# Performance work log

Measured on AMD Instinct MI355X. Metric: run time of the kernel, lower is better.

The kernel has to match this reference:

```python
import jax, jax.numpy as jnp
import numpy as np

GROUPS = 1024
K_N = 32
FEAT_DIM = 64
EPS = 1e-05


def farthest_point_sample(xyz, npoint):
    # xyz: [B, N, 3] -> centroids [B, npoint] int32
    # Original torch code starts from a random point; we use index 0 for determinism.
    B, N, _ = xyz.shape

    def step(carry, _):
        distance, farthest = carry
        centroid = jnp.take_along_axis(xyz, farthest[:, None, None], axis=1)  # [B,1,3]
        dist = jnp.sum((xyz - centroid) ** 2, axis=-1)  # [B,N]
        distance = jnp.minimum(distance, dist)
        new_far = jnp.argmax(distance, axis=-1).astype(jnp.int32)
        return (distance, new_far), farthest

    init = (jnp.full((B, N), 1e10, dtype=xyz.dtype), jnp.zeros((B,), jnp.int32))
    _, cents = jax.lax.scan(step, init, None, length=npoint)
    return cents.T  # [B, npoint]


def index_points(points, idx):
    # points: [B, N, C]; idx: [B, ...] -> [B, ..., C]
    B = points.shape[0]
    bidx = jnp.arange(B).reshape((B,) + (1,) * (idx.ndim - 1))
    return points[bidx, idx]


def square_distance(src, dst):
    # src [B,S,C], dst [B,N,C] -> [B,S,N]
    d = -2.0 * jnp.einsum('bsc,bnc->bsn', src, dst)
    d = d + jnp.sum(src ** 2, -1)[:, :, None]
    d = d + jnp.sum(dst ** 2, -1)[:, None, :]
    return d


def setup_inputs() -> dict:
    key = jax.random.key(0)
    k1, k2 = jax.random.split(key)
    xyz = jax.random.normal(k1, (8, 3, 4096), dtype=jnp.float32)
    feats = jax.random.normal(k2, (8, FEAT_DIM, 4096), dtype=jnp.float32)
    affine_alpha_p = jnp.ones((1, 1, 1, FEAT_DIM), jnp.float32)
    affine_beta_p = jnp.zeros((1, 1, 1, FEAT_DIM), jnp.float32)
    return {"xyz": xyz, "feats": feats,
            "affine_alpha_p": affine_alpha_p, "affine_beta_p": affine_beta_p}


def reference(xyz, feats, affine_alpha_p, affine_beta_p):
    xyz = jnp.transpose(xyz, (0, 2, 1))      # [B,N,3]
    feats = jnp.transpose(feats, (0, 2, 1))  # [B,N,D]
    B, N, _ = xyz.shape
    S, k = GROUPS, K_N

    fps_idx = farthest_point_sample(xyz, S)          # [B,S]
    new_xyz = index_points(xyz, fps_idx)             # [B,S,3]
    new_feats = index_points(feats, fps_idx)         # [B,S,D]

    sqr = square_distance(new_xyz, xyz)              # [B,S,N]
    _, idx = jax.lax.top_k(-sqr, k)                  # smallest-k -> [B,S,k]
    grouped = index_points(feats, idx)               # [B,S,k,D]

    mean = new_feats[:, :, None, :]                  # [B,S,1,D]
    diff = grouped - mean
    # torch.std over flattened per-batch, unbiased (ddof=1)
    std = jnp.std(diff.reshape(B, -1), axis=-1, ddof=1)[:, None, None, None]
    grouped = diff / (std + EPS)
    grouped = affine_alpha_p * grouped + affine_beta_p

    point_feats = jnp.concatenate(
        [grouped, grouped - new_feats[:, :, None, :]], axis=-1)  # [B,S,k,2D]

    new_feats_out = jnp.transpose(new_feats, (0, 2, 1))          # [B,D,S]
    new_xyz_out = jnp.transpose(new_xyz, (0, 2, 1))              # [B,3,S]
    point_feats_out = jnp.transpose(point_feats, (0, 3, 1, 2))   # [B,2D,S,k]
    return (new_xyz_out, new_feats_out, point_feats_out)
```

## Files before the change

### kernel.cpp

```cpp
#include <hip/hip_runtime.h>

#define NPTS 4096
#define NSAMP 1024
#define KNN_K 32
#define FDIM 64
#define EPSF 1e-5f

typedef float v2f __attribute__((ext_vector_type(2)));

#define DPP_MAX64(CTRL)                                                          \
  {                                                                              \
    unsigned _olo = (unsigned)__builtin_amdgcn_update_dpp(0, (int)klo, CTRL,     \
                                                          0xf, 0xf, true);       \
    unsigned _ohi = (unsigned)__builtin_amdgcn_update_dpp(0, (int)khi, CTRL,     \
                                                          0xf, 0xf, true);       \
    unsigned long long _ok = ((unsigned long long)_ohi << 32) | _olo;            \
    unsigned long long _ck = ((unsigned long long)khi << 32) | klo;              \
    if (_ok > _ck) { klo = _olo; khi = _ohi; }                                   \
  }

__global__ __launch_bounds__(512) void fps_kernel(const float* __restrict__ xyz,
                                                  int* __restrict__ fps_idx,
                                                  float* __restrict__ sqnorm,
                                                  float* __restrict__ out0,
                                                  float4* __restrict__ nx4) {
#pragma clang fp contract(off)
  __shared__ float4 pts[NPTS];
  __shared__ unsigned long long skeys[2][8];
  __shared__ int fpsb[NSAMP];
  const int b = blockIdx.x, t = threadIdx.x;
  const int lane = t & 63, w = t >> 6;
  const float* xb = xyz + (size_t)b * 3 * NPTS;
  v2f px[4], py[4], pz[4], dst[4];
#pragma unroll
  for (int j = 0; j < 4; ++j) {
    int p0 = (2 * j) * 512 + t, p1 = (2 * j + 1) * 512 + t;
    float x0 = xb[p0], y0 = xb[NPTS + p0], z0 = xb[2 * NPTS + p0];
    float x1 = xb[p1], y1 = xb[NPTS + p1], z1 = xb[2 * NPTS + p1];
    float sq0 = __fadd_rn(__fadd_rn(__fmul_rn(x0, x0), __fmul_rn(y0, y0)),
                          __fmul_rn(z0, z0));
    float sq1 = __fadd_rn(__fadd_rn(__fmul_rn(x1, x1), __fmul_rn(y1, y1)),
                          __fmul_rn(z1, z1));
    pts[p0] = make_float4(x0, y0, z0, sq0);
    pts[p1] = make_float4(x1, y1, z1, sq1);
    sqnorm[b * NPTS + p0] = sq0;
    sqnorm[b * NPTS + p1] = sq1;
    px[j].x = x0; px[j].y = x1;
    py[j].x = y0; py[j].y = y1;
    pz[j].x = z0; pz[j].y = z1;
    dst[j].x = 1e10f;
    dst[j].y = 1e10f;
  }
  if (t == 0) { fps_idx[b * NSAMP] = 0; fpsb[0] = 0; }
  __syncthreads();
  float4 c = pts[0];
  for (int it = 1; it < NSAMP; ++it) {
    v2f vcx, vcy, vcz;
    vcx.x = c.x; vcx.y = c.x;
    vcy.x = c.y; vcy.y = c.y;
    vcz.x = c.z; vcz.y = c.z;
#pragma unroll
    for (int j = 0; j < 4; ++j) {
      v2f dx = px[j] - vcx;
      v2f dy = py[j] - vcy;
      v2f dz = pz[j] - vcz;
      v2f dd = (dx * dx + dy * dy) + dz * dz;
      dst[j].x = fminf(dst[j].x, dd.x);
      dst[j].y = fminf(dst[j].y, dd.y);
    }
    float bv = -1.0f;
    int bi = 0;
#pragma unroll
    for (int k = 0; k < 8; ++k) {
      float nd = (k & 1) ? dst[k >> 1].y : dst[k >> 1].x;
      int n = k * 512 + t;
      if (nd > bv) { bv = nd; bi = n; }
    }
    unsigned bvb = __float_as_uint(bv);
    unsigned klo = (bvb << 12) | (unsigned)(4095 - bi);
    unsigned khi = bvb >> 20;
    DPP_MAX64(0x111)
    DPP_MAX64(0x112)
    DPP_MAX64(0x114)
    DPP_MAX64(0x118)
    DPP_MAX64(0x142)
    DPP_MAX64(0x143)
    const int buf = it & 1;
    if (lane == 63) skeys[buf][w] = ((unsigned long long)khi << 32) | klo;
    __syncthreads();
    unsigned long long kk = skeys[buf][lane & 7];
    klo = (unsigned)kk;
    khi = (unsigned)(kk >> 32);
    DPP_MAX64(0x111)
    DPP_MAX64(0x112)
    DPP_MAX64(0x114)
    unsigned flo = (unsigned)__builtin_amdgcn_readlane((int)klo, 7);
    int far = 4095 - (int)(flo & 0xfffu);
    if (t == 0) { fps_idx[b * NSAMP + it] = far; fpsb[it] = far; }
    c = pts[far];
  }
  __syncthreads();
#pragma unroll
  for (int k = 0; k < 2; ++k) {
    int s = k * 512 + t;
    int p = fpsb[s];
    float4 q = pts[p];
    out0[(b * 3 + 0) * 1024 + s] = q.x;
    out0[(b * 3 + 1) * 1024 + s] = q.y;
    out0[(b * 3 + 2) * 1024 + s] = q.z;
    nx4[b * 1024 + s] = q;
  }
}

__global__ __launch_bounds__(256) void gather_feats_kernel(const float* __restrict__ feats,
                                                           const int* __restrict__ fps,
                                                           float* __restrict__ out1,
                                                           float* __restrict__ nf) {
  int i = blockIdx.x * 256 + threadIdx.x;
  int s = i & 1023, c = (i >> 10) & 63, b = i >> 16;
  int p = fps[(b << 10) + s];
  float v = feats[((size_t)(b * 64 + c)) * NPTS + p];
  out1[(b * 64 + c) * 1024 + s] = v;
  nf[(((b << 10) + s) << 6) + c] = v;
}

__device__ __forceinline__ unsigned long long mk_key(float xn, float yn, float zn,
                                                     float sq, float cx, float cy,
                                                     float cz, float src2, int n) {
  float dot = __fmaf_rn(zn, cz, __fmaf_rn(yn, cy, __fmul_rn(xn, cx)));
  float d = __fadd_rn(__fadd_rn(__fmul_rn(-2.0f, dot), src2), sq);
  unsigned mb = __float_as_uint(d);
  mb = (mb & 0x80000000u) ? ~mb : (mb | 0x80000000u);
  return ((unsigned long long)mb << 32) | (unsigned)n;
}

__global__ __launch_bounds__(256, 2) void knn_kernel(const float* __restrict__ xyz,
                                                     const float* __restrict__ sqnorm,
                                                     const float4* __restrict__ nx4,
                                                     int* __restrict__ knn) {
  const int lane = threadIdx.x & 63;
  const int w = threadIdx.x >> 6;
  const int row = blockIdx.x * 4 + w;
  const int b = row >> 10;
  const float4 c4 = nx4[row];
  const float cx = c4.x, cy = c4.y, cz = c4.z, src2 = c4.w;
  const float4* x4 = (const float4*)(xyz + (size_t)b * 3 * NPTS);
  const float4* y4 = (const float4*)(xyz + (size_t)b * 3 * NPTS + NPTS);
  const float4* z4 = (const float4*)(xyz + (size_t)b * 3 * NPTS + 2 * NPTS);
  const float4* s4 = (const float4*)(sqnorm + (size_t)b * NPTS);
  unsigned long long key[64];
#pragma unroll
  for (int jj = 0; jj < 16; ++jj) {
    int vi = jj * 64 + lane;
    float4 xv = x4[vi], yv = y4[vi], zv = z4[vi], sv = s4[vi];
    int n0 = vi * 4;
    key[jj * 4 + 0] = mk_key(xv.x, yv.x, zv.x, sv.x, cx, cy, cz, src2, n0);
    key[jj * 4 + 1] = mk_key(xv.y, yv.y, zv.y, sv.y, cx, cy, cz, src2, n0 + 1);
    key[jj * 4 + 2] = mk_key(xv.z, yv.z, zv.z, sv.z, cx, cy, cz, src2, n0 + 2);
    key[jj * 4 + 3] = mk_key(xv.w, yv.w, zv.w, sv.w, cx, cy, cz, src2, n0 + 3);
  }
  unsigned long long last = 0ull;
  const int out_base = row * KNN_K;
#pragma unroll 1
  for (int r = 0; r < KNN_K; ++r) {
    unsigned long long cur = ~0ull;
#pragma unroll
    for (int j = 0; j < 64; ++j) {
      unsigned long long k = key[j];
      if (k > last && k < cur) cur = k;
    }
#pragma unroll
    for (int off = 32; off > 0; off >>= 1) {
      unsigned long long o = __shfl_xor(cur, off);
      cur = (o < cur) ? o : cur;
    }
    last = cur;
    if (lane == r) knn[out_base + r] = (int)(unsigned)(cur & 0xffffffffull);
  }
}

__global__ __launch_bounds__(256) void stats_kernel(const float* __restrict__ feats,
                                                    const float* __restrict__ nf,
                                                    const int* __restrict__ knn,
                                                    double* __restrict__ stats) {
  const int b = blockIdx.x >> 5;
  const int chunk = blockIdx.x & 31;
  const int base = chunk * 65536;
  double sm = 0.0, sq = 0.0;
  for (int i = 0; i < 256; ++i) {
    int e = base + i * 256 + threadIdx.x;
    int c = e >> 15;
    int sk = e & 32767;
    int s = sk >> 5, j = sk & 31;
    int p = knn[((((b << 10) + s)) << 5) + j];
    float f = feats[((size_t)(b * 64 + c)) * NPTS + p];
    float m = nf[(((b << 10) + s) << 6) + c];
    double d = (double)__fsub_rn(f, m);
    sm += d;
    sq += d * d;
  }
#pragma unroll
  for (int off = 32; off > 0; off >>= 1) {
    sm += __shfl_down(sm, off);
    sq += __shfl_down(sq, off);
  }
  __shared__ double red[8];
  int w = threadIdx.x >> 6;
  if ((threadIdx.x & 63) == 0) { red[w * 2] = sm; red[w * 2 + 1] = sq; }
  __syncthreads();
  if (threadIdx.x == 0) {
    atomicAdd(&stats[b * 2 + 0], red[0] + red[2] + red[4] + red[6]);
    atomicAdd(&stats[b * 2 + 1], red[1] + red[3] + red[5] + red[7]);
  }
}

__global__ __launch_bounds__(256) void out_kernel(const float* __restrict__ feats,
                                                  const float* __restrict__ nf,
                                                  const int* __restrict__ knn,
                                                  const double* __restrict__ stats,
                                                  const float* __restrict__ alpha,
                                                  const float* __restrict__ beta,
                                                  float* __restrict__ out2) {
  const int plane = blockIdx.x;
  const int b = plane >> 6, c = plane & 63;
  const int sk = blockIdx.y * 256 + threadIdx.x;
  const int s = sk >> 5, j = sk & 31;
  const double n = 2097152.0;
  double sm = stats[b * 2], sqs = stats[b * 2 + 1];
  double var = (sqs - sm * sm / n) / (n - 1.0);
  float stdf = (float)sqrt(var);
  float denom = stdf + EPSF;
  int p = knn[((((b << 10) + s)) << 5) + j];
  float f = feats[((size_t)(b * 64 + c)) * NPTS + p];
  float m = nf[(((b << 10) + s) << 6) + c];
  float diff = __fsub_rn(f, m);
  float g = alpha[c] * (diff / denom) + beta[c];
  size_t o1 = (((size_t)(b * 128 + c) << 10) + (size_t)s) * 32 + j;
  size_t o2 = (((size_t)(b * 128 + 64 + c) << 10) + (size_t)s) * 32 + j;
  out2[o1] = g;
  out2[o2] = g - m;
}

extern "C" void kernel_launch(void* const* d_in, const int* in_sizes, int n_in,
                              void* d_out, int out_size, void* d_ws, size_t ws_size,
                              hipStream_t stream) {
  (void)in_sizes; (void)n_in; (void)out_size; (void)ws_size;
  const float* xyz   = (const float*)d_in[0];
  const float* feats = (const float*)d_in[1];
  const float* alpha = (const float*)d_in[2];
  const float* beta  = (const float*)d_in[3];
  float* out  = (float*)d_out;
  float* out0 = out;
  float* out1 = out + 24576;
  float* out2 = out + 24576 + 524288;

  char* ws = (char*)d_ws;
  int*    fps   = (int*)ws;
  float*  sqn   = (float*)(ws + 32768);
  float4* nx4   = (float4*)(ws + 163840);
  float*  nf    = (float*)(ws + 294912);
  int*    knn   = (int*)(ws + 2392064);
  double* stats = (double*)(ws + 3440640);

  hipMemsetAsync(stats, 0, 128, stream);
  fps_kernel<<<8, 512, 0, stream>>>(xyz, fps, sqn, out0, nx4);
  gather_feats_kernel<<<2048, 256, 0, stream>>>(feats, fps, out1, nf);
  knn_kernel<<<2048, 256, 0, stream>>>(xyz, sqn, nx4, knn);
  stats_kernel<<<256, 256, 0, stream>>>(feats, nf, knn, stats);
  out_kernel<<<dim3(512, 128), 256, 0, stream>>>(feats, nf, knn, stats, alpha, beta, out2);
}
```

Measured before the change: 977.0 us.

## Merge knn and feature gather into one launch, vectorize stats and output kernels

Merges the feature-gather kernel into the knn kernel as extra blocks so there is one fewer launch and the gather can overlap with knn work. Vectorizes the gather, stats and output kernels to handle four elements per thread with int4/float4 loads and stores, and replaces the per-element divide with a reciprocal multiply. The stats kernel now accumulates per thread in float rather than double before the double reduction, which may change numerical accuracy. The knn kernel also drops its launch_bounds minimum of two blocks per CU, which can change register allocation and occupancy.

```diff
diff --git a/kernel.cpp b/kernel.cpp
--- a/kernel.cpp
+++ b/kernel.cpp
@@ -112,18 +112,6 @@
   }
 }
 
-__global__ __launch_bounds__(256) void gather_feats_kernel(const float* __restrict__ feats,
-                                                           const int* __restrict__ fps,
-                                                           float* __restrict__ out1,
-                                                           float* __restrict__ nf) {
-  int i = blockIdx.x * 256 + threadIdx.x;
-  int s = i & 1023, c = (i >> 10) & 63, b = i >> 16;
-  int p = fps[(b << 10) + s];
-  float v = feats[((size_t)(b * 64 + c)) * NPTS + p];
-  out1[(b * 64 + c) * 1024 + s] = v;
-  nf[(((b << 10) + s) << 6) + c] = v;
-}
-
 __device__ __forceinline__ unsigned long long mk_key(float xn, float yn, float zn,
                                                      float sq, float cx, float cy,
                                                      float cz, float src2, int n) {
@@ -134,48 +122,66 @@
   return ((unsigned long long)mb << 32) | (unsigned)n;
 }
 
-__global__ __launch_bounds__(256, 2) void knn_kernel(const float* __restrict__ xyz,
-                                                     const float* __restrict__ sqnorm,
-                                                     const float4* __restrict__ nx4,
-                                                     int* __restrict__ knn) {
-  const int lane = threadIdx.x & 63;
-  const int w = threadIdx.x >> 6;
-  const int row = blockIdx.x * 4 + w;
-  const int b = row >> 10;
-  const float4 c4 = nx4[row];
-  const float cx = c4.x, cy = c4.y, cz = c4.z, src2 = c4.w;
-  const float4* x4 = (const float4*)(xyz + (size_t)b * 3 * NPTS);
-  const float4* y4 = (const float4*)(xyz + (size_t)b * 3 * NPTS + NPTS);
-  const float4* z4 = (const float4*)(xyz + (size_t)b * 3 * NPTS + 2 * NPTS);
-  const float4* s4 = (const float4*)(sqnorm + (size_t)b * NPTS);
-  unsigned long long key[64];
-#pragma unroll
-  for (int jj = 0; jj < 16; ++jj) {
-    int vi = jj * 64 + lane;
-    float4 xv = x4[vi], yv = y4[vi], zv = z4[vi], sv = s4[vi];
-    int n0 = vi * 4;
-    key[jj * 4 + 0] = mk_key(xv.x, yv.x, zv.x, sv.x, cx, cy, cz, src2, n0);
-    key[jj * 4 + 1] = mk_key(xv.y, yv.y, zv.y, sv.y, cx, cy, cz, src2, n0 + 1);
-    key[jj * 4 + 2] = mk_key(xv.z, yv.z, zv.z, sv.z, cx, cy, cz, src2, n0 + 2);
-    key[jj * 4 + 3] = mk_key(xv.w, yv.w, zv.w, sv.w, cx, cy, cz, src2, n0 + 3);
-  }
-  unsigned long long last = 0ull;
-  const int out_base = row * KNN_K;
+__global__ __launch_bounds__(256) void mid_kernel(const float* __restrict__ xyz,
+                                                  const float* __restrict__ sqnorm,
+                                                  const float4* __restrict__ nx4,
+                                                  int* __restrict__ knn,
+                                                  const float* __restrict__ feats,
+                                                  const int* __restrict__ fps,
+                                                  float* __restrict__ out1,
+                                                  float* __restrict__ nf) {
+  if (blockIdx.x < 2048) {
+    const int lane = threadIdx.x & 63;
+    const int w = threadIdx.x >> 6;
+    const int row = blockIdx.x * 4 + w;
+    const int b = row >> 10;
+    const float4 c4 = nx4[row];
+    const float cx = c4.x, cy = c4.y, cz = c4.z, src2 = c4.w;
+    const float4* x4 = (const float4*)(xyz + (size_t)b * 3 * NPTS);
+    const float4* y4 = (const float4*)(xyz + (size_t)b * 3 * NPTS + NPTS);
+    const float4* z4 = (const float4*)(xyz + (size_t)b * 3 * NPTS + 2 * NPTS);
+    const float4* s4 = (const float4*)(sqnorm + (size_t)b * NPTS);
+    unsigned long long key[64];
+#pragma unroll
+    for (int jj = 0; jj < 16; ++jj) {
+      int vi = jj * 64 + lane;
+      float4 xv = x4[vi], yv = y4[vi], zv = z4[vi], sv = s4[vi];
+      int n0 = vi * 4;
+      key[jj * 4 + 0] = mk_key(xv.x, yv.x, zv.x, sv.x, cx, cy, cz, src2, n0);
+      key[jj * 4 + 1] = mk_key(xv.y, yv.y, zv.y, sv.y, cx, cy, cz, src2, n0 + 1);
+      key[jj * 4 + 2] = mk_key(xv.z, yv.z, zv.z, sv.z, cx, cy, cz, src2, n0 + 2);
+      key[jj * 4 + 3] = mk_key(xv.w, yv.w, zv.w, sv.w, cx, cy, cz, src2, n0 + 3);
+    }
+    unsigned long long last = 0ull;
+    const int out_base = row * KNN_K;
 #pragma unroll 1
-  for (int r = 0; r < KNN_K; ++r) {
-    unsigned long long cur = ~0ull;
-#pragma unroll
-    for (int j = 0; j < 64; ++j) {
-      unsigned long long k = key[j];
-      if (k > last && k < cur) cur = k;
-    }
-#pragma unroll
-    for (int off = 32; off > 0; off >>= 1) {
-      unsigned long long o = __shfl_xor(cur, off);
-      cur = (o < cur) ? o : cur;
-    }
-    last = cur;
-    if (lane == r) knn[out_base + r] = (int)(unsigned)(cur & 0xffffffffull);
+    for (int r = 0; r < KNN_K; ++r) {
+      unsigned long long cur = ~0ull;
+#pragma unroll
+      for (int j = 0; j < 64; ++j) {
+        unsigned long long k = key[j];
+        if (k > last && k < cur) cur = k;
+      }
+#pragma unroll
+      for (int off = 32; off > 0; off >>= 1) {
+        unsigned long long o = __shfl_xor(cur, off);
+        cur = (o < cur) ? o : cur;
+      }
+      last = cur;
+      if (lane == r) knn[out_base + r] = (int)(unsigned)(cur & 0xffffffffull);
+    }
+  } else {
+    int i = (blockIdx.x - 2048) * 256 + threadIdx.x;
+    int s4i = i & 255, c = (i >> 8) & 63, b = i >> 14;
+    int s0 = s4i * 4;
+    const int4 p = *(const int4*)&fps[(b << 10) + s0];
+    const float* fc = feats + (size_t)(b * 64 + c) * NPTS;
+    float v0 = fc[p.x], v1 = fc[p.y], v2 = fc[p.z], v3 = fc[p.w];
+    *(float4*)&out1[(b * 64 + c) * 1024 + s0] = make_float4(v0, v1, v2, v3);
+    nf[(((b << 10) + s0 + 0) << 6) + c] = v0;
+    nf[(((b << 10) + s0 + 1) << 6) + c] = v1;
+    nf[(((b << 10) + s0 + 2) << 6) + c] = v2;
+    nf[(((b << 10) + s0 + 3) << 6) + c] = v3;
   }
 }
 
@@ -185,28 +191,32 @@
                                                     double* __restrict__ stats) {
   const int b = blockIdx.x >> 5;
   const int chunk = blockIdx.x & 31;
-  const int base = chunk * 65536;
-  double sm = 0.0, sq = 0.0;
-  for (int i = 0; i < 256; ++i) {
-    int e = base + i * 256 + threadIdx.x;
-    int c = e >> 15;
-    int sk = e & 32767;
-    int s = sk >> 5, j = sk & 31;
-    int p = knn[((((b << 10) + s)) << 5) + j];
-    float f = feats[((size_t)(b * 64 + c)) * NPTS + p];
+  const float* fb = feats + (size_t)b * 64 * NPTS;
+  float sm = 0.0f, sq = 0.0f;
+  for (int it = 0; it < 64; ++it) {
+    int e0 = chunk * 65536 + (it * 256 + threadIdx.x) * 4;
+    int c = e0 >> 15;
+    int sk = e0 & 32767;
+    int s = sk >> 5, j0 = sk & 31;
+    const int4 pq = *(const int4*)&knn[(((b << 10) + s) << 5) + j0];
     float m = nf[(((b << 10) + s) << 6) + c];
-    double d = (double)__fsub_rn(f, m);
-    sm += d;
-    sq += d * d;
-  }
+    const float* fc = fb + (size_t)c * NPTS;
+    float d0 = __fsub_rn(fc[pq.x], m);
+    float d1 = __fsub_rn(fc[pq.y], m);
+    float d2 = __fsub_rn(fc[pq.z], m);
+    float d3 = __fsub_rn(fc[pq.w], m);
+    sm += (d0 + d1) + (d2 + d3);
+    sq = fmaf(d0, d0, fmaf(d1, d1, fmaf(d2, d2, fmaf(d3, d3, sq))));
+  }
+  double dsm = (double)sm, dsq = (double)sq;
 #pragma unroll
   for (int off = 32; off > 0; off >>= 1) {
-    sm += __shfl_down(sm, off);
-    sq += __shfl_down(sq, off);
+    dsm += __shfl_down(dsm, off);
+    dsq += __shfl_down(dsq, off);
   }
   __shared__ double red[8];
   int w = threadIdx.x >> 6;
-  if ((threadIdx.x & 63) == 0) { red[w * 2] = sm; red[w * 2 + 1] = sq; }
+  if ((threadIdx.x & 63) == 0) { red[w * 2] = dsm; red[w * 2 + 1] = dsq; }
   __syncthreads();
   if (threadIdx.x == 0) {
     atomicAdd(&stats[b * 2 + 0], red[0] + red[2] + red[4] + red[6]);
@@ -223,22 +233,25 @@
                                                   float* __restrict__ out2) {
   const int plane = blockIdx.x;
   const int b = plane >> 6, c = plane & 63;
-  const int sk = blockIdx.y * 256 + threadIdx.x;
-  const int s = sk >> 5, j = sk & 31;
   const double n = 2097152.0;
   double sm = stats[b * 2], sqs = stats[b * 2 + 1];
   double var = (sqs - sm * sm / n) / (n - 1.0);
-  float stdf = (float)sqrt(var);
-  float denom = stdf + EPSF;
-  int p = knn[((((b << 10) + s)) << 5) + j];
-  float f = feats[((size_t)(b * 64 + c)) * NPTS + p];
+  float denom = (float)sqrt(var) + EPSF;
+  float inv = 1.0f / denom;
+  float al = alpha[c], be = beta[c];
+  int sk0 = (blockIdx.y * 256 + threadIdx.x) * 4;
+  int s = sk0 >> 5, j0 = sk0 & 31;
+  const int4 pq = *(const int4*)&knn[(((b << 10) + s) << 5) + j0];
+  const float* fc = feats + (size_t)(b * 64 + c) * NPTS;
   float m = nf[(((b << 10) + s) << 6) + c];
-  float diff = __fsub_rn(f, m);
-  float g = alpha[c] * (diff / denom) + beta[c];
-  size_t o1 = (((size_t)(b * 128 + c) << 10) + (size_t)s) * 32 + j;
-  size_t o2 = (((size_t)(b * 128 + 64 + c) << 10) + (size_t)s) * 32 + j;
-  out2[o1] = g;
-  out2[o2] = g - m;
+  float g0 = al * (__fsub_rn(fc[pq.x], m) * inv) + be;
+  float g1 = al * (__fsub_rn(fc[pq.y], m) * inv) + be;
+  float g2 = al * (__fsub_rn(fc[pq.z], m) * inv) + be;
+  float g3 = al * (__fsub_rn(fc[pq.w], m) * inv) + be;
+  size_t o1 = (((size_t)(b * 128 + c) << 10) + (size_t)s) * 32 + j0;
+  size_t o2 = (((size_t)(b * 128 + 64 + c) << 10) + (size_t)s) * 32 + j0;
+  *(float4*)&out2[o1] = make_float4(g0, g1, g2, g3);
+  *(float4*)&out2[o2] = make_float4(g0 - m, g1 - m, g2 - m, g3 - m);
 }
 
 extern "C" void kernel_launch(void* const* d_in, const int* in_sizes, int n_in,
@@ -264,8 +277,7 @@
 
   hipMemsetAsync(stats, 0, 128, stream);
   fps_kernel<<<8, 512, 0, stream>>>(xyz, fps, sqn, out0, nx4);
-  gather_feats_kernel<<<2048, 256, 0, stream>>>(feats, fps, out1, nf);
-  knn_kernel<<<2048, 256, 0, stream>>>(xyz, sqn, nx4, knn);
+  mid_kernel<<<2560, 256, 0, stream>>>(xyz, sqn, nx4, knn, feats, fps, out1, nf);
   stats_kernel<<<256, 256, 0, stream>>>(feats, nf, knn, stats);
-  out_kernel<<<dim3(512, 128), 256, 0, stream>>>(feats, nf, knn, stats, alpha, beta, out2);
-}
+  out_kernel<<<dim3(512, 32), 256, 0, stream>>>(feats, nf, knn, stats, alpha, beta, out2);
+}
```

Result: no change. 958.8 us (-1.9%).
